# Kernel tuning notes

Measured on AMD Instinct MI355X. Metric: run time of the kernel, lower is better.

The kernel has to match this reference:

```python
import jax, jax.numpy as jnp
import numpy as np

HIDDEN = 2048
HEADS = 16
HEAD_DIM = HIDDEN // HEADS
BATCH = 2
SEQ = 2048
LN_EPS = 1e-5


def setup_inputs() -> dict:
    key = jax.random.key(0)
    ks = jax.random.split(key, 14)
    g = 0.02  # xavier gain used in _init_weights
    lim = g * np.sqrt(6.0 / (HIDDEN + HIDDEN))
    def lin_w(k):
        return jax.random.uniform(k, (HIDDEN, HIDDEN), jnp.float32, -lim, lim)
    inp = {
        "hidden_states": jax.random.normal(ks[0], (BATCH, SEQ, HIDDEN), jnp.float32),
        "cross_states": jax.random.normal(ks[1], (BATCH, SEQ, HIDDEN), jnp.float32),
        "Wq": lin_w(ks[2]), "bq": jnp.zeros((HIDDEN,), jnp.float32),
        "Wk": lin_w(ks[3]), "bk": jnp.zeros((HIDDEN,), jnp.float32),
        "Wv": lin_w(ks[4]), "bv": jnp.zeros((HIDDEN,), jnp.float32),
        "Wo": lin_w(ks[5]), "bo": jnp.zeros((HIDDEN,), jnp.float32),
        "Wg": jax.random.uniform(ks[6], (HIDDEN, HIDDEN), jnp.float32, -np.sqrt(6.0/(2*HIDDEN)), np.sqrt(6.0/(2*HIDDEN))),
        "bg": jnp.zeros((HIDDEN,), jnp.float32),
        "ln_gamma": jnp.ones((HIDDEN,), jnp.float32),
        "ln_beta": jnp.zeros((HIDDEN,), jnp.float32),
    }
    return inp


def reference(hidden_states, cross_states, Wq, bq, Wk, bk, Wv, bv, Wo, bo, Wg, bg, ln_gamma, ln_beta):
    B, S, H = hidden_states.shape
    scale = HEAD_DIM ** -0.5
    # projections (weights stored as [in, out]; equivalent to torch x @ W.T with W.T pre-applied)
    q = hidden_states @ Wq + bq
    k = cross_states @ Wk + bk
    v = cross_states @ Wv + bv
    # [B, S, H] -> [B, heads, S, head_dim]
    def split_heads(x):
        return x.reshape(B, -1, HEADS, HEAD_DIM).transpose(0, 2, 1, 3)
    q, k, v = split_heads(q), split_heads(k), split_heads(v)
    scores = jnp.einsum('bhqd,bhkd->bhqk', q, k) * scale
    probs = jax.nn.softmax(scores, axis=-1)
    attn = jnp.einsum('bhqk,bhkd->bhqd', probs, v)
    attn = attn.transpose(0, 2, 1, 3).reshape(B, -1, H)
    attn = attn @ Wo + bo
    gate = jax.nn.sigmoid(hidden_states @ Wg + bg)
    attn = gate * attn  # dropout rate 0 -> identity
    out = hidden_states + attn
    mu = jnp.mean(out, axis=-1, keepdims=True)
    var = jnp.mean(jnp.square(out - mu), axis=-1, keepdims=True)
    out = (out - mu) * jax.lax.rsqrt(var + LN_EPS) * ln_gamma + ln_beta
    return out
```

## Files before the change

kernel.cpp:

```cpp
#include <hip/hip_runtime.h>

typedef __bf16 bf16;
typedef bf16 bf16x8 __attribute__((ext_vector_type(8)));
typedef bf16 bf16x4 __attribute__((ext_vector_type(4)));
typedef float floatx4 __attribute__((ext_vector_type(4)));

#define HID 2048
#define MROWS 4096

__device__ __forceinline__ void gload_lds16(const bf16* g, bf16* l) {
    __builtin_amdgcn_global_load_lds((const __attribute__((address_space(1))) void*)g,
                                     (__attribute__((address_space(3))) void*)l, 16, 0, 0);
}

__global__ __launch_bounds__(256) void convert2_kernel(const float* __restrict__ X0, const float* __restrict__ X1,
                                                       bf16* __restrict__ Y0, bf16* __restrict__ Y1)
{
    const float* X = blockIdx.z ? X1 : X0;
    bf16* Y = blockIdx.z ? Y1 : Y0;
    const int i = (blockIdx.x * 256 + threadIdx.x) * 4;
    const float4 v = *(const float4*)(X + i);
    bf16x4 o;
    o[0] = (bf16)v.x; o[1] = (bf16)v.y; o[2] = (bf16)v.z; o[3] = (bf16)v.w;
    *(bf16x4*)(Y + i) = o;
}

__global__ __launch_bounds__(256) void transpose5_kernel(
    const float* __restrict__ W0, const float* __restrict__ W1, const float* __restrict__ W2,
    const float* __restrict__ W3, const float* __restrict__ W4,
    bf16* __restrict__ T0, bf16* __restrict__ T1, bf16* __restrict__ T2,
    bf16* __restrict__ T3, bf16* __restrict__ T4)
{
    const float* W; bf16* WT;
    switch (blockIdx.z) {
        case 0: W = W0; WT = T0; break;
        case 1: W = W1; WT = T1; break;
        case 2: W = W2; WT = T2; break;
        case 3: W = W3; WT = T3; break;
        default: W = W4; WT = T4; break;
    }
    __shared__ float tile[32][33];
    const int n0 = blockIdx.x * 32, k0 = blockIdx.y * 32;
    const int tx = threadIdx.x & 31, ty = threadIdx.x >> 5;
    #pragma unroll
    for (int r = 0; r < 32; r += 8)
        tile[ty + r][tx] = W[(size_t)(k0 + ty + r) * HID + n0 + tx];
    __syncthreads();
    #pragma unroll
    for (int r = 0; r < 32; r += 8)
        WT[(size_t)(n0 + ty + r) * HID + k0 + tx] = (bf16)tile[tx][ty + r];
}

__global__ __launch_bounds__(256) void transpose_v_kernel(const bf16* __restrict__ X, bf16* __restrict__ Y)
{
    __shared__ bf16 tile[32][33];
    const int b = blockIdx.z;
    const int c0 = blockIdx.x * 32, t0 = blockIdx.y * 32;
    const int tx = threadIdx.x & 31, ty = threadIdx.x >> 5;
    const bf16* Xb = X + (size_t)b * HID * HID;
    bf16* Yb = Y + (size_t)b * HID * HID;
    #pragma unroll
    for (int r = 0; r < 32; r += 8)
        tile[ty + r][tx] = Xb[(size_t)(t0 + ty + r) * HID + c0 + tx];
    __syncthreads();
    #pragma unroll
    for (int r = 0; r < 32; r += 8)
        Yb[(size_t)(c0 + ty + r) * HID + t0 + tx] = tile[tx][ty + r];
}

__global__ __launch_bounds__(256) void gemm_qgkv_kernel(const bf16* __restrict__ H, const bf16* __restrict__ Cx,
                                                        const bf16* __restrict__ Wqg, const bf16* __restrict__ Wkv,
                                                        const float* __restrict__ bq, const float* __restrict__ bg,
                                                        const float* __restrict__ bk, const float* __restrict__ bv,
                                                        bf16* __restrict__ qo, bf16* __restrict__ go,
                                                        bf16* __restrict__ ko, bf16* __restrict__ vo)
{
    constexpr int BK = 64;
    __shared__ __align__(16) bf16 As[128 * BK];
    __shared__ __align__(16) bf16 Bs[128 * BK];
    const int z = blockIdx.z;
    const bf16* A  = z ? Cx : H;
    const bf16* BT = z ? Wkv : Wqg;
    const int tid = threadIdx.x;
    const int wave = tid >> 6, lane = tid & 63;
    const int m0 = blockIdx.x * 128, n0 = blockIdx.y * 128;
    const int wm = (wave & 1) * 64, wn = (wave >> 1) * 64;
    const int l15 = lane & 15, q = lane >> 4;
    const int swz = l15 & 7;
    floatx4 acc[4][4] = {};

    const int srow = tid >> 3;
    const int scc = ((tid & 7) ^ (srow & 7)) * 8;
    const bf16* Ag = A  + (size_t)(m0 + srow) * HID + scc;
    const bf16* Bg = BT + (size_t)(n0 + srow) * HID + scc;
    bf16* Asl = As + tid * 8;
    bf16* Bsl = Bs + tid * 8;

    for (int kt = 0; kt < HID; kt += BK) {
        __syncthreads();
        #pragma unroll
        for (int rr = 0; rr < 4; rr++) {
            gload_lds16(Ag + (size_t)(rr * 32) * HID + kt, Asl + rr * 2048);
            gload_lds16(Bg + (size_t)(rr * 32) * HID + kt, Bsl + rr * 2048);
        }
        __syncthreads();
        #pragma unroll
        for (int ks = 0; ks < 2; ks++) {
            const int cc = (ks * 4 + q) ^ swz;
            bf16x8 af[4], bfr[4];
            #pragma unroll
            for (int i = 0; i < 4; i++)
                af[i] = *(const bf16x8*)(As + (wm + i * 16 + l15) * 64 + cc * 8);
            #pragma unroll
            for (int j = 0; j < 4; j++)
                bfr[j] = *(const bf16x8*)(Bs + (wn + j * 16 + l15) * 64 + cc * 8);
            #pragma unroll
            for (int i = 0; i < 4; i++)
                #pragma unroll
                for (int j = 0; j < 4; j++)
                    acc[i][j] = __builtin_amdgcn_mfma_f32_16x16x32_bf16(af[i], bfr[j], acc[i][j], 0, 0, 0);
        }
    }
    const bool half2 = (n0 >= HID);
    const float* bias = z ? (half2 ? bv : bk) : (half2 ? bg : bq);
    bf16* C = z ? (half2 ? vo : ko) : (half2 ? go : qo);
    const bool sig = (!z) && half2;
    const int nb = n0 - (half2 ? HID : 0);
    #pragma unroll
    for (int j = 0; j < 4; j++) {
        const int col = nb + wn + j * 16 + l15;
        const float bvv = bias[col];
        #pragma unroll
        for (int i = 0; i < 4; i++) {
            #pragma unroll
            for (int r = 0; r < 4; r++) {
                const int row = m0 + wm + i * 16 + q * 4 + r;
                float val = acc[i][j][r] + bvv;
                if (sig) val = 1.0f / (1.0f + __expf(-val));
                C[(size_t)row * HID + col] = (bf16)val;
            }
        }
    }
}

__global__ __launch_bounds__(256) void gemm_bt_kernel(const bf16* __restrict__ A, const bf16* __restrict__ BT,
                                                      const float* __restrict__ bias, bf16* __restrict__ C)
{
    constexpr int BK = 64;
    __shared__ __align__(16) bf16 As[128 * BK];
    __shared__ __align__(16) bf16 Bs[128 * BK];
    const int tid = threadIdx.x;
    const int wave = tid >> 6, lane = tid & 63;
    const int m0 = blockIdx.x * 128, n0 = blockIdx.y * 128;
    const int wm = (wave & 1) * 64, wn = (wave >> 1) * 64;
    const int l15 = lane & 15, q = lane >> 4;
    const int swz = l15 & 7;
    floatx4 acc[4][4] = {};
    const int srow = tid >> 3;
    const int scc = ((tid & 7) ^ (srow & 7)) * 8;
    const bf16* Ag = A  + (size_t)(m0 + srow) * HID + scc;
    const bf16* Bg = BT + (size_t)(n0 + srow) * HID + scc;
    bf16* Asl = As + tid * 8;
    bf16* Bsl = Bs + tid * 8;

    for (int kt = 0; kt < HID; kt += BK) {
        __syncthreads();
        #pragma unroll
        for (int rr = 0; rr < 4; rr++) {
            gload_lds16(Ag + (size_t)(rr * 32) * HID + kt, Asl + rr * 2048);
            gload_lds16(Bg + (size_t)(rr * 32) * HID + kt, Bsl + rr * 2048);
        }
        __syncthreads();
        #pragma unroll
        for (int ks = 0; ks < 2; ks++) {
            const int cc = (ks * 4 + q) ^ swz;
            bf16x8 af[4], bfr[4];
            #pragma unroll
            for (int i = 0; i < 4; i++)
                af[i] = *(const bf16x8*)(As + (wm + i * 16 + l15) * 64 + cc * 8);
            #pragma unroll
            for (int j = 0; j < 4; j++)
                bfr[j] = *(const bf16x8*)(Bs + (wn + j * 16 + l15) * 64 + cc * 8);
            #pragma unroll
            for (int i = 0; i < 4; i++)
                #pragma unroll
                for (int j = 0; j < 4; j++)
                    acc[i][j] = __builtin_amdgcn_mfma_f32_16x16x32_bf16(af[i], bfr[j], acc[i][j], 0, 0, 0);
        }
    }
    #pragma unroll
    for (int j = 0; j < 4; j++) {
        const int col = n0 + wn + j * 16 + l15;
        const float bvv = bias[col];
        #pragma unroll
        for (int i = 0; i < 4; i++) {
            #pragma unroll
            for (int r = 0; r < 4; r++) {
                const int row = m0 + wm + i * 16 + q * 4 + r;
                C[(size_t)row * HID + col] = (bf16)(acc[i][j][r] + bvv);
            }
        }
    }
}

__global__ __launch_bounds__(256) void attention_mfma4_kernel(const bf16* __restrict__ Q, const bf16* __restrict__ K,
                                                              const bf16* __restrict__ Vt,
                                                              bf16* __restrict__ Op0, bf16* __restrict__ Op1,
                                                              float* __restrict__ lp0, float* __restrict__ lp1)
{
    constexpr int PP = 72;
    __shared__ __align__(16) bf16 Ks[64 * 128];
    __shared__ __align__(16) bf16 Vts[128 * 64];
    __shared__ __align__(16) bf16 Ps[128 * PP];

    const int tid = threadIdx.x;
    const int wave = tid >> 6, lane = tid & 63;
    const int l15 = lane & 15, quad = lane >> 4;
    const int swz = l15 & 7;
    const int b = blockIdx.x >> 4, h = blockIdx.x & 15;
    const int q0 = blockIdx.y * 128;
    const int kt0 = blockIdx.z * 1024;
    bf16* Op = blockIdx.z ? Op1 : Op0;
    float* lp = blockIdx.z ? lp1 : lp0;
    const bf16* Qg = Q + (size_t)(b * 2048) * HID + h * 128;
    const bf16* Kg = K + (size_t)b * 2048 * HID + h * 128;
    const bf16* Vg = Vt + (size_t)(b * 2048 + h * 128) * HID;

    const int wq0 = wave * 32;

    const float qsc = 0.08838834764831845f * 1.44269504f;
    bf16x8 qreg[2][4];
    #pragma unroll
    for (int s = 0; s < 2; s++)
        #pragma unroll
        for (int kk = 0; kk < 4; kk++) {
            bf16x8 t = *(const bf16x8*)(Qg + (size_t)(q0 + wq0 + s * 16 + l15) * HID + kk * 32 + quad * 8);
            #pragma unroll
            for (int e = 0; e < 8; e++) t[e] = (bf16)((float)t[e] * qsc);
            qreg[s][kk] = t;
        }

    const int krow = tid >> 4;
    const int kcc = ((tid & 15) ^ (krow & 7)) * 8;
    const bf16* KgS = Kg + (size_t)krow * HID + kcc;
    bf16* Ksl = Ks + tid * 8;
    const int vrow = tid >> 3;
    const int vcc = ((tid & 7) ^ (vrow & 7)) * 8;
    const bf16* VgS = Vg + (size_t)vrow * HID + vcc;
    bf16* Vsl = Vts + tid * 8;

    float lsum[2] = {0.f, 0.f};
    floatx4 oacc[2][8] = {};

    for (int kt = kt0; kt < kt0 + 1024; kt += 64) {
        __syncthreads();
        #pragma unroll
        for (int rr = 0; rr < 4; rr++) {
            gload_lds16(KgS + (size_t)(kt + rr * 16) * HID, Ksl + rr * 2048);
            gload_lds16(VgS + (size_t)(rr * 32) * HID + kt, Vsl + rr * 2048);
        }
        __syncthreads();

        floatx4 sacc[4][2];
        #pragma unroll
        for (int j = 0; j < 4; j++)
            #pragma unroll
            for (int s = 0; s < 2; s++) sacc[j][s] = (floatx4){0.f, 0.f, 0.f, 0.f};
        #pragma unroll
        for (int kk = 0; kk < 4; kk++) {
            const int cc = (kk * 4 + quad) ^ swz;
            #pragma unroll
            for (int j = 0; j < 4; j++) {
                const bf16x8 kf = *(const bf16x8*)(Ks + (j * 16 + l15) * 128 + cc * 8);
                #pragma unroll
                for (int s = 0; s < 2; s++)
                    sacc[j][s] = __builtin_amdgcn_mfma_f32_16x16x32_bf16(kf, qreg[s][kk], sacc[j][s], 0, 0, 0);
            }
        }

        #pragma unroll
        for (int s = 0; s < 2; s++) {
            const int prow = wq0 + s * 16 + l15;
            float ps = 0.f;
            #pragma unroll
            for (int j = 0; j < 4; j++) {
                bf16x4 pw;
                #pragma unroll
                for (int r = 0; r < 4; r++) {
                    const float p = exp2f(sacc[j][s][r]);
                    ps += p;
                    pw[r] = (bf16)p;
                }
                *(bf16x4*)(Ps + prow * PP + j * 16 + quad * 4) = pw;
            }
            lsum[s] += ps;
        }
        #pragma unroll
        for (int ks = 0; ks < 2; ks++) {
            const int cc = (ks * 4 + quad) ^ swz;
            bf16x8 pf[2];
            #pragma unroll
            for (int s = 0; s < 2; s++)
                pf[s] = *(const bf16x8*)(Ps + (wq0 + s * 16 + l15) * PP + ks * 32 + quad * 8);
            #pragma unroll
            for (int dt = 0; dt < 8; dt++) {
                const bf16x8 vf = *(const bf16x8*)(Vts + (dt * 16 + l15) * 64 + cc * 8);
                #pragma unroll
                for (int s = 0; s < 2; s++)
                    oacc[s][dt] = __builtin_amdgcn_mfma_f32_16x16x32_bf16(pf[s], vf, oacc[s][dt], 0, 0, 0);
            }
        }
    }

    #pragma unroll
    for (int s = 0; s < 2; s++) {
        float l = lsum[s];
        l += __shfl_xor(l, 16);
        l += __shfl_xor(l, 32);
        if (quad == 0)
            lp[(size_t)(b * 2048 + q0 + wq0 + s * 16 + l15) * 16 + h] = l;
        #pragma unroll
        for (int r = 0; r < 4; r++) {
            const size_t row = (size_t)(b * 2048 + q0 + wq0 + s * 16 + quad * 4 + r);
            #pragma unroll
            for (int dt = 0; dt < 8; dt++)
                Op[row * HID + h * 128 + dt * 16 + l15] = (bf16)(oacc[s][dt][r]);
        }
    }
}

__global__ __launch_bounds__(256) void attn_combine_kernel(const bf16* __restrict__ O0, const bf16* __restrict__ O1,
                                                           const float* __restrict__ l0, const float* __restrict__ l1,
                                                           bf16* __restrict__ out)
{
    const int row = blockIdx.x;
    const int c0 = threadIdx.x * 8;
    const int h = c0 >> 7;
    const size_t base = (size_t)row * HID;
    const float inv = 1.f / (l0[row * 16 + h] + l1[row * 16 + h]);
    const bf16x8 a = *(const bf16x8*)(O0 + base + c0);
    const bf16x8 c = *(const bf16x8*)(O1 + base + c0);
    bf16x8 o;
    #pragma unroll
    for (int e = 0; e < 8; e++) o[e] = (bf16)(((float)a[e] + (float)c[e]) * inv);
    *(bf16x8*)(out + base + c0) = o;
}

__global__ __launch_bounds__(256) void ln_kernel(const float* __restrict__ hidden, const bf16* __restrict__ gate,
                                                 const bf16* __restrict__ attnp, const float* __restrict__ gamma,
                                                 const float* __restrict__ beta, float* __restrict__ out)
{
    __shared__ float red[4];
    __shared__ float red2[4];
    const int row = blockIdx.x;
    const int tid = threadIdx.x;
    const size_t base = (size_t)row * HID;
    const int c0 = tid * 8;
    const float4 h0 = *(const float4*)(hidden + base + c0);
    const float4 h1 = *(const float4*)(hidden + base + c0 + 4);
    const bf16x8 g = *(const bf16x8*)(gate + base + c0);
    const bf16x8 a = *(const bf16x8*)(attnp + base + c0);
    float t[8] = {h0.x, h0.y, h0.z, h0.w, h1.x, h1.y, h1.z, h1.w};
    float sum = 0.f;
    #pragma unroll
    for (int e = 0; e < 8; e++) { t[e] += (float)g[e] * (float)a[e]; sum += t[e]; }
    #pragma unroll
    for (int o = 1; o < 64; o <<= 1) sum += __shfl_xor(sum, o);
    const int wave = tid >> 6, lane = tid & 63;
    if (lane == 0) red[wave] = sum;
    __syncthreads();
    const float mu = (red[0] + red[1] + red[2] + red[3]) * (1.f / HID);
    float vs = 0.f;
    #pragma unroll
    for (int e = 0; e < 8; e++) { const float d = t[e] - mu; vs += d * d; }
    #pragma unroll
    for (int o = 1; o < 64; o <<= 1) vs += __shfl_xor(vs, o);
    if (lane == 0) red2[wave] = vs;
    __syncthreads();
    const float var = (red2[0] + red2[1] + red2[2] + red2[3]) * (1.f / HID);
    const float inv = rsqrtf(var + 1e-5f);
    float res[8];
    #pragma unroll
    for (int e = 0; e < 8; e++) res[e] = (t[e] - mu) * inv * gamma[c0 + e] + beta[c0 + e];
    *(float4*)(out + base + c0)     = make_float4(res[0], res[1], res[2], res[3]);
    *(float4*)(out + base + c0 + 4) = make_float4(res[4], res[5], res[6], res[7]);
}

extern "C" void kernel_launch(void* const* d_in, const int* in_sizes, int n_in,
                              void* d_out, int out_size, void* d_ws, size_t ws_size,
                              hipStream_t stream) {
    const float* hidden = (const float*)d_in[0];
    const float* cross  = (const float*)d_in[1];
    const float* Wq = (const float*)d_in[2];
    const float* bq = (const float*)d_in[3];
    const float* Wk = (const float*)d_in[4];
    const float* bk = (const float*)d_in[5];
    const float* Wv = (const float*)d_in[6];
    const float* bv = (const float*)d_in[7];
    const float* Wo = (const float*)d_in[8];
    const float* bo = (const float*)d_in[9];
    const float* Wg = (const float*)d_in[10];
    const float* bg = (const float*)d_in[11];
    const float* gamma = (const float*)d_in[12];
    const float* beta  = (const float*)d_in[13];
    float* out = (float*)d_out;

    char* ws = (char*)d_ws;
    const size_t MB = 1ull << 20;
    bf16* hbf  = (bf16*)(ws);
    bf16* cbf  = (bf16*)(ws + 16 * MB);
    bf16* WqgT = (bf16*)(ws + 32 * MB);
    bf16* WkvT = (bf16*)(ws + 48 * MB);
    bf16* WoT  = (bf16*)(ws + 64 * MB);
    bf16* qbf  = (bf16*)(ws + 72 * MB);
    bf16* kbf  = (bf16*)(ws + 88 * MB);
    bf16* vbf  = (bf16*)(ws + 104 * MB);
    bf16* gbf  = (bf16*)(ws + 120 * MB);
    bf16* abf  = (bf16*)(ws + 136 * MB);
    bf16* WgTp = WqgT + (size_t)HID * HID;
    bf16* WvTp = WkvT + (size_t)HID * HID;
    bf16* vtr  = cbf;
    bf16* Op0  = hbf;
    bf16* Op1  = WqgT;
    float* l0  = (float*)WkvT;
    float* l1  = (float*)((char*)WkvT + 1 * MB);
    bf16* pbf  = qbf;

    convert2_kernel<<<dim3(8192, 1, 2), 256, 0, stream>>>(hidden, cross, hbf, cbf);
    transpose5_kernel<<<dim3(64, 64, 5), 256, 0, stream>>>(Wq, Wg, Wk, Wv, Wo, WqgT, WgTp, WkvT, WvTp, WoT);
    gemm_qgkv_kernel<<<dim3(32, 32, 2), 256, 0, stream>>>(hbf, cbf, WqgT, WkvT, bq, bg, bk, bv,
                                                          qbf, gbf, kbf, vbf);
    transpose_v_kernel<<<dim3(64, 64, 2), 256, 0, stream>>>(vbf, vtr);
    attention_mfma4_kernel<<<dim3(32, 16, 2), 256, 0, stream>>>(qbf, kbf, vtr, Op0, Op1, l0, l1);
    attn_combine_kernel<<<MROWS, 256, 0, stream>>>(Op0, Op1, l0, l1, abf);
    gemm_bt_kernel<<<dim3(32, 16), 256, 0, stream>>>(abf, WoT, bo, pbf);
    ln_kernel<<<MROWS, 256, 0, stream>>>(hidden, gbf, pbf, gamma, beta, out);
}
```

Measured before the change: 511.3 us.

## Rewrite QGKV projection GEMM as 256x256 tile with multi-stage LDS pipeline

Replaces the 128x128 single-buffered fused Q/gate/K/V GEMM with a 256x256-tile, 512-thread kernel. Each K step is split into four quadrants, and global-to-LDS loads for later K steps are issued while MFMAs run on the current one, using explicit vmcnt/lgkmcnt waits, barriers and setprio. The larger tile increases data reuse per loaded byte and the staging hides load latency. In exchange it uses much more LDS (128KB), more registers, and fewer blocks (512), which risks lower occupancy and tail effects.

```diff
diff --git a/kernel.cpp b/kernel.cpp
--- a/kernel.cpp
+++ b/kernel.cpp
@@ -68,74 +68,144 @@
         Yb[(size_t)(c0 + ty + r) * HID + t0 + tx] = tile[tx][ty + r];
 }
 
-__global__ __launch_bounds__(256) void gemm_qgkv_kernel(const bf16* __restrict__ H, const bf16* __restrict__ Cx,
-                                                        const bf16* __restrict__ Wqg, const bf16* __restrict__ Wkv,
-                                                        const float* __restrict__ bq, const float* __restrict__ bg,
-                                                        const float* __restrict__ bk, const float* __restrict__ bv,
-                                                        bf16* __restrict__ qo, bf16* __restrict__ go,
-                                                        bf16* __restrict__ ko, bf16* __restrict__ vo)
+#define BAR() __builtin_amdgcn_s_barrier()
+#define WAIT_LGKM0() asm volatile("s_waitcnt lgkmcnt(0)" ::: "memory")
+#define WAIT_VM(N) asm volatile("s_waitcnt vmcnt(" #N ")" ::: "memory")
+
+#define READ_A(SLOT) do { \
+    _Pragma("unroll") \
+    for (int mf = 0; mf < 4; mf++) \
+      _Pragma("unroll") \
+      for (int ks = 0; ks < 2; ks++) \
+        af[mf][ks] = *(const bf16x8*)((SLOT) + (wm + mf * 16 + l15) * 64 + (((ks * 4 + quad) ^ swz) * 8)); \
+    } while (0)
+
+#define READ_B(DST, SLOT) do { \
+    _Pragma("unroll") \
+    for (int nf = 0; nf < 2; nf++) \
+      _Pragma("unroll") \
+      for (int ks = 0; ks < 2; ks++) \
+        DST[nf][ks] = *(const bf16x8*)((SLOT) + (wn + nf * 16 + l15) * 64 + (((ks * 4 + quad) ^ swz) * 8)); \
+    } while (0)
+
+#define STAGE_A(DSTSLOT, ROWOFF, KT) do { \
+    gload_lds16(Asrc + (size_t)(ROWOFF) * HID + (KT),        (DSTSLOT) + ldsOff); \
+    gload_lds16(Asrc + (size_t)((ROWOFF) + 64) * HID + (KT), (DSTSLOT) + ldsOff + 4096); } while (0)
+
+#define STAGE_B(DSTSLOT, ROWOFF, KT) do { \
+    gload_lds16(Bsrc + (size_t)(ROWOFF) * HID + (KT),        (DSTSLOT) + ldsOff); \
+    gload_lds16(Bsrc + (size_t)((ROWOFF) + 64) * HID + (KT), (DSTSLOT) + ldsOff + 4096); } while (0)
+
+#define MFMA_QUAD(BF, MH, NH) \
+    __builtin_amdgcn_s_setprio(1); \
+    _Pragma("unroll") \
+    for (int ks = 0; ks < 2; ks++) \
+      _Pragma("unroll") \
+      for (int mf = 0; mf < 4; mf++) \
+        _Pragma("unroll") \
+        for (int nf = 0; nf < 2; nf++) \
+          acc[(MH) * 4 + mf][(NH) * 2 + nf] = __builtin_amdgcn_mfma_f32_16x16x32_bf16( \
+              af[mf][ks], BF[nf][ks], acc[(MH) * 4 + mf][(NH) * 2 + nf], 0, 0, 0); \
+    __builtin_amdgcn_s_setprio(0);
+
+__global__ __launch_bounds__(512, 2) void gemm_qgkv256_kernel(
+    const bf16* __restrict__ H, const bf16* __restrict__ Cx,
+    const bf16* __restrict__ Wqg, const bf16* __restrict__ Wkv,
+    const float* __restrict__ bq, const float* __restrict__ bg,
+    const float* __restrict__ bk, const float* __restrict__ bv,
+    bf16* __restrict__ qo, bf16* __restrict__ go,
+    bf16* __restrict__ ko, bf16* __restrict__ vo)
 {
     constexpr int BK = 64;
-    __shared__ __align__(16) bf16 As[128 * BK];
-    __shared__ __align__(16) bf16 Bs[128 * BK];
+    constexpr int NT = HID / BK;
+    __shared__ __align__(16) bf16 Ar[4][128 * BK];
+    __shared__ __align__(16) bf16 Br[4][128 * BK];
+
     const int z = blockIdx.z;
     const bf16* A  = z ? Cx : H;
     const bf16* BT = z ? Wkv : Wqg;
     const int tid = threadIdx.x;
     const int wave = tid >> 6, lane = tid & 63;
-    const int m0 = blockIdx.x * 128, n0 = blockIdx.y * 128;
-    const int wm = (wave & 1) * 64, wn = (wave >> 1) * 64;
-    const int l15 = lane & 15, q = lane >> 4;
+    const int m0 = blockIdx.x * 256, n0 = blockIdx.y * 256;
+    const int wm = (wave & 1) * 64;
+    const int wn = (wave >> 1) * 32;
+    const int l15 = lane & 15, quad = lane >> 4;
     const int swz = l15 & 7;
-    floatx4 acc[4][4] = {};
-
-    const int srow = tid >> 3;
-    const int scc = ((tid & 7) ^ (srow & 7)) * 8;
-    const bf16* Ag = A  + (size_t)(m0 + srow) * HID + scc;
-    const bf16* Bg = BT + (size_t)(n0 + srow) * HID + scc;
-    bf16* Asl = As + tid * 8;
-    bf16* Bsl = Bs + tid * 8;
-
-    for (int kt = 0; kt < HID; kt += BK) {
-        __syncthreads();
-        #pragma unroll
-        for (int rr = 0; rr < 4; rr++) {
-            gload_lds16(Ag + (size_t)(rr * 32) * HID + kt, Asl + rr * 2048);
-            gload_lds16(Bg + (size_t)(rr * 32) * HID + kt, Bsl + rr * 2048);
-        }
-        __syncthreads();
-        #pragma unroll
-        for (int ks = 0; ks < 2; ks++) {
-            const int cc = (ks * 4 + q) ^ swz;
-            bf16x8 af[4], bfr[4];
-            #pragma unroll
-            for (int i = 0; i < 4; i++)
-                af[i] = *(const bf16x8*)(As + (wm + i * 16 + l15) * 64 + cc * 8);
-            #pragma unroll
-            for (int j = 0; j < 4; j++)
-                bfr[j] = *(const bf16x8*)(Bs + (wn + j * 16 + l15) * 64 + cc * 8);
-            #pragma unroll
-            for (int i = 0; i < 4; i++)
-                #pragma unroll
-                for (int j = 0; j < 4; j++)
-                    acc[i][j] = __builtin_amdgcn_mfma_f32_16x16x32_bf16(af[i], bfr[j], acc[i][j], 0, 0, 0);
-        }
-    }
+
+    floatx4 acc[8][4] = {};
+
+    const int hrow = tid >> 3;
+    const int cc0  = (tid & 7) ^ (hrow & 7);
+    const bf16* Asrc = A  + (size_t)(m0 + hrow) * HID + cc0 * 8;
+    const bf16* Bsrc = BT + (size_t)(n0 + hrow) * HID + cc0 * 8;
+    const int ldsOff = tid * 8;
+
+    STAGE_A(Ar[0], 0,   0);
+    STAGE_B(Br[0], 0,   0);
+    STAGE_A(Ar[1], 128, 0);
+    STAGE_B(Br[1], 128, 0);
+    STAGE_A(Ar[2], 0,   BK);
+    STAGE_B(Br[2], 0,   BK);
+    WAIT_VM(4); BAR();
+
+    bf16x8 af[4][2], bl[2][2], bh[2][2];
+    READ_B(bl, Br[0]);
+
+    for (int t = 0; t < NT; t++) {
+        const int sw = (t & 1) << 1;
+        bf16* a_lo   = Ar[sw];
+        bf16* a_hi   = Ar[sw | 1];
+        bf16* b_hi   = Br[sw | 1];
+        bf16* a_hi_n = Ar[(sw | 1) ^ 2];
+        bf16* b_hi_n = Br[(sw | 1) ^ 2];
+        bf16* b_lo_n = Br[sw ^ 2];
+        const int kt1 = (t + 1) * BK, kt2 = (t + 2) * BK;
+        const bool g1 = (t + 1 < NT), g2 = (t + 2 < NT);
+
+        READ_A(a_lo);
+        if (g1) STAGE_A(a_hi_n, 128, kt1);
+        BAR(); WAIT_LGKM0();
+        MFMA_QUAD(bl, 0, 0);
+        WAIT_VM(6); BAR();
+
+        READ_B(bh, b_hi);
+        if (g1) STAGE_B(b_hi_n, 128, kt1);
+        BAR(); WAIT_LGKM0();
+        MFMA_QUAD(bh, 0, 1);
+        WAIT_VM(6); BAR();
+
+        READ_A(a_hi);
+        if (g2) STAGE_A(Ar[sw], 0, kt2);
+        BAR(); WAIT_LGKM0();
+        MFMA_QUAD(bl, 1, 0);
+        WAIT_VM(6); BAR();
+
+        if (g1) READ_B(bl, b_lo_n);
+        if (g2) STAGE_B(Br[sw], 0, kt2);
+        BAR(); WAIT_LGKM0();
+        MFMA_QUAD(bh, 1, 1);
+        WAIT_VM(6); BAR();
+    }
+
     const bool half2 = (n0 >= HID);
     const float* bias = z ? (half2 ? bv : bk) : (half2 ? bg : bq);
     bf16* C = z ? (half2 ? vo : ko) : (half2 ? go : qo);
     const bool sig = (!z) && half2;
     const int nb = n0 - (half2 ? HID : 0);
     #pragma unroll
-    for (int j = 0; j < 4; j++) {
-        const int col = nb + wn + j * 16 + l15;
+    for (int nh = 0; nh < 2; nh++)
+    #pragma unroll
+    for (int nf = 0; nf < 2; nf++) {
+        const int col = nb + nh * 128 + wn + nf * 16 + l15;
         const float bvv = bias[col];
         #pragma unroll
-        for (int i = 0; i < 4; i++) {
+        for (int mh = 0; mh < 2; mh++)
+        #pragma unroll
+        for (int mf = 0; mf < 4; mf++) {
             #pragma unroll
             for (int r = 0; r < 4; r++) {
-                const int row = m0 + wm + i * 16 + q * 4 + r;
-                float val = acc[i][j][r] + bvv;
+                const int row = m0 + mh * 128 + wm + mf * 16 + quad * 4 + r;
+                float val = acc[mh * 4 + mf][nh * 2 + nf][r] + bvv;
                 if (sig) val = 1.0f / (1.0f + __expf(-val));
                 C[(size_t)row * HID + col] = (bf16)val;
             }
@@ -428,8 +498,8 @@
 
     convert2_kernel<<<dim3(8192, 1, 2), 256, 0, stream>>>(hidden, cross, hbf, cbf);
     transpose5_kernel<<<dim3(64, 64, 5), 256, 0, stream>>>(Wq, Wg, Wk, Wv, Wo, WqgT, WgTp, WkvT, WvTp, WoT);
-    gemm_qgkv_kernel<<<dim3(32, 32, 2), 256, 0, stream>>>(hbf, cbf, WqgT, WkvT, bq, bg, bk, bv,
-                                                          qbf, gbf, kbf, vbf);
+    gemm_qgkv256_kernel<<<dim3(16, 16, 2), 512, 0, stream>>>(hbf, cbf, WqgT, WkvT, bq, bg, bk, bv,
+                                                             qbf, gbf, kbf, vbf);
     transpose_v_kernel<<<dim3(64, 64, 2), 256, 0, stream>>>(vbf, vtr);
     attention_mfma4_kernel<<<dim3(32, 16, 2), 256, 0, stream>>>(qbf, kbf, vtr, Op0, Op1, l0, l1);
     attn_combine_kernel<<<MROWS, 256, 0, stream>>>(Op0, Op1, l0, l1, abf);
```

New measurement: 483.1 us. -5.5%, faster.
